# Kernel tuning notes

Measured on AMD Instinct MI355X. Metric: run time of the kernel, lower is better.

Reference implementation:

```python
import jax, jax.numpy as jnp
import numpy as np

B, SQ, SK = 2, 2048, 2048
D = 1024            # in_features == num_heads * head_size
H, HS = 16, 64      # num_heads, head_size
SCALE = HS ** -0.5


def setup_inputs() -> dict:
    key = jax.random.key(0)
    ks = jax.random.split(key, 10)
    s = 0.02
    return {
        "inputs": jax.random.normal(ks[0], (B, SQ, D), jnp.float32),
        "context": jax.random.normal(ks[1], (B, SK, D), jnp.float32),
        "Wq": jax.random.normal(ks[2], (D, D), jnp.float32) * s,
        "bq": jnp.zeros((D,), jnp.float32),
        "Wk": jax.random.normal(ks[3], (D, D), jnp.float32) * s,
        "bk": jnp.zeros((D,), jnp.float32),
        "Wv": jax.random.normal(ks[4], (D, D), jnp.float32) * s,
        "bv": jnp.zeros((D,), jnp.float32),
        "Wo": jax.random.normal(ks[5], (D, D), jnp.float32) * s,
        "bo": jnp.zeros((D,), jnp.float32),
    }


def reference(inputs, context, Wq, bq, Wk, bk, Wv, bv, Wo, bo):
    # QKV projections (torch Linear: x @ W.T + b; here W stored as [in, out])
    q = inputs @ Wq + bq            # [B, SQ, D]
    k = context @ Wk + bk           # [B, SK, D]
    v = context @ Wv + bv           # [B, SK, D]
    q = q.reshape(B, SQ, H, HS)
    k = k.reshape(B, SK, H, HS)
    v = v.reshape(B, SK, H, HS)
    # scores: [B, H, SQ, SK] -- full score matrix materialized (as in source)
    score = jnp.einsum("bqhd,bkhd->bhqk", q, k) * SCALE
    weights = jax.nn.softmax(score, axis=-1)
    attn = jnp.einsum("bhqk,bkhd->bqhd", weights, v)  # [B, SQ, H, HS]
    out = attn.reshape(B, SQ, H * HS)
    return out @ Wo + bo
```

## Files before the change

kernel.cpp:

```cpp
#include <hip/hip_runtime.h>

#define BB 2
#define SQ 2048
#define SK 2048
#define DD 1024
#define HH 16
#define HS 64
#define SCALE 0.125f
#define LOG2E 1.4426950408889634f

typedef __bf16 bf16x8 __attribute__((ext_vector_type(8)));
typedef float f32x4 __attribute__((ext_vector_type(4)));
typedef unsigned int uint;

#if defined(__has_builtin)
#if __has_builtin(__builtin_amdgcn_exp2f)
#define FEXP2(x) __builtin_amdgcn_exp2f(x)
#endif
#endif
#ifndef FEXP2
extern "C" __device__ float __ocml_native_exp2_f32(float);
#define FEXP2(x) __ocml_native_exp2_f32(x)
#endif

__device__ __forceinline__ void gload_lds16(const __bf16* g, __bf16* l) {
    __builtin_amdgcn_global_load_lds((const __attribute__((address_space(1))) uint*)(g),
                                     (__attribute__((address_space(3))) uint*)(l), 16, 0, 0);
}

__global__ void cast2_f32_bf16(const float* __restrict__ in0, const float* __restrict__ in1,
                               __bf16* __restrict__ out0, __bf16* __restrict__ out1, int n8each) {
    int i = blockIdx.x * blockDim.x + threadIdx.x;
    const float* src;
    __bf16* dst;
    int j;
    if (i < n8each) { src = in0; dst = out0; j = i; }
    else            { src = in1; dst = out1; j = i - n8each; }
    const float4* p = ((const float4*)src) + (size_t)j * 2;
    float4 a = p[0], b = p[1];
    bf16x8 v = {(__bf16)a.x, (__bf16)a.y, (__bf16)a.z, (__bf16)a.w,
                (__bf16)b.x, (__bf16)b.y, (__bf16)b.z, (__bf16)b.w};
    ((bf16x8*)dst)[j] = v;
}

__global__ void wtrans(const float* __restrict__ W0, const float* __restrict__ W1,
                       const float* __restrict__ W2, const float* __restrict__ W3,
                       __bf16* __restrict__ Wt) {
    __shared__ __bf16 tile[32][33];
    const float* W = blockIdx.z == 0 ? W0 : blockIdx.z == 1 ? W1 : blockIdx.z == 2 ? W2 : W3;
    __bf16* out = Wt + (size_t)blockIdx.z * DD * DD;
    int tx = threadIdx.x, ty = threadIdx.y;
    int k0 = blockIdx.y * 32, n0 = blockIdx.x * 32;
#pragma unroll
    for (int j = 0; j < 4; ++j)
        tile[ty + j * 8][tx] = (__bf16)W[(size_t)(k0 + ty + j * 8) * DD + n0 + tx];
    __syncthreads();
#pragma unroll
    for (int j = 0; j < 4; ++j) {
        int n = n0 + ty + j * 8;
        int k = k0 + tx;
        int kswz = (k & ~63) | ((((k >> 3) ^ n) & 7) << 3) | (k & 7);
        out[(size_t)n * DD + kswz] = tile[tx][ty + j * 8];
    }
}

__global__ __launch_bounds__(256) void gemm_qkv(
        const __bf16* __restrict__ Ain, const __bf16* __restrict__ Actx,
        const __bf16* __restrict__ Wt,
        const float* __restrict__ bq, const float* __restrict__ bk, const float* __restrict__ bv,
        __bf16* __restrict__ Qb, __bf16* __restrict__ Kb, __bf16* __restrict__ Vtb,
        float qscale) {
    __shared__ __bf16 As[128 * 64];
    __shared__ __bf16 Bs[128 * 64];
    int t = threadIdx.x, w = t >> 6, l = t & 63;
    int lm = l & 15, lk = l >> 4;
    int wr = w >> 1, wc = w & 1;
    int flat = blockIdx.x + 16 * blockIdx.y;
    int nf = (flat & 7) * 96 + (flat >> 3);
    bool isQ = nf < 256;
    int bc, br;
    if (isQ) { bc = nf & 7; br = nf >> 3; }
    else     { int f = nf - 256; bc = f & 15; br = f >> 4; }

    int rA = t >> 3, cA = t & 7;
    const __bf16* ag = (isQ ? Ain : Actx) + (size_t)(br * 128 + rA) * 1024 + ((cA ^ (rA & 7)) * 8);
    __bf16* adst = &As[rA * 64 + cA * 8];
    const __bf16 *bg0, *bg1, *bg2, *bg3;
    if (isQ) {
        const __bf16* Wq_ = Wt;
        bg0 = Wq_ + (size_t)(bc * 128 + rA)      * 1024 + cA * 8;
        bg1 = Wq_ + (size_t)(bc * 128 + rA + 32) * 1024 + cA * 8;
        bg2 = Wq_ + (size_t)(bc * 128 + rA + 64) * 1024 + cA * 8;
        bg3 = Wq_ + (size_t)(bc * 128 + rA + 96) * 1024 + cA * 8;
    } else {
        const __bf16* Wk_ = Wt + (size_t)DD * DD;
        const __bf16* Wv_ = Wt + (size_t)2 * DD * DD;
        bg0 = Wk_ + (size_t)(bc * 64 + rA)      * 1024 + cA * 8;
        bg1 = Wk_ + (size_t)(bc * 64 + rA + 32) * 1024 + cA * 8;
        bg2 = Wv_ + (size_t)(bc * 64 + rA)      * 1024 + cA * 8;
        bg3 = Wv_ + (size_t)(bc * 64 + rA + 32) * 1024 + cA * 8;
    }
    __bf16* bdst = &Bs[rA * 64 + cA * 8];

    int brow[4];
#pragma unroll
    for (int n = 0; n < 4; ++n)
        brow[n] = isQ ? (wc * 64 + n * 16 + lm)
                      : ((n >> 1) * 64 + wc * 32 + (n & 1) * 16 + lm);

#define STAGE(KT)                                                                     \
    gload_lds16(ag + (KT),               adst);                                       \
    gload_lds16(ag + 32768 + (KT),       adst + 2048);                                \
    gload_lds16(ag + 65536 + (KT),       adst + 4096);                                \
    gload_lds16(ag + 98304 + (KT),       adst + 6144);                                \
    gload_lds16(bg0 + (KT), bdst);                                                    \
    gload_lds16(bg1 + (KT), bdst + 2048);                                             \
    gload_lds16(bg2 + (KT), bdst + 4096);                                             \
    gload_lds16(bg3 + (KT), bdst + 6144);

    f32x4 acc[4][4] = {};
    for (int ts = 0; ts < 16; ++ts) {
        __syncthreads();
        STAGE(ts * 64);
        __syncthreads();
#pragma unroll
        for (int kk = 0; kk < 2; ++kk) {
            int ch = kk * 4 + lk;
            bf16x8 af[4], bf[4];
#pragma unroll
            for (int m = 0; m < 4; ++m)
                af[m] = *(const bf16x8*)&As[(wr * 64 + m * 16 + lm) * 64 + ((ch ^ (lm & 7)) * 8)];
#pragma unroll
            for (int n = 0; n < 4; ++n)
                bf[n] = *(const bf16x8*)&Bs[brow[n] * 64 + ((ch ^ (lm & 7)) * 8)];
#pragma unroll
            for (int m = 0; m < 4; ++m)
#pragma unroll
                for (int n = 0; n < 4; ++n)
                    acc[m][n] = __builtin_amdgcn_mfma_f32_16x16x32_bf16(af[m], bf[n], acc[m][n], 0, 0, 0);
        }
    }
#undef STAGE

    if (isQ) {
#pragma unroll
        for (int m = 0; m < 4; ++m)
#pragma unroll
            for (int n = 0; n < 4; ++n) {
                int col = bc * 128 + wc * 64 + n * 16 + lm;
                float bb = bq[col];
#pragma unroll
                for (int r = 0; r < 4; ++r) {
                    int row = br * 128 + wr * 64 + m * 16 + lk * 4 + r;
                    Qb[(size_t)row * 1024 + col] = (__bf16)((acc[m][n][r] + bb) * qscale);
                }
            }
    } else {
#pragma unroll
        for (int m = 0; m < 4; ++m)
#pragma unroll
            for (int n = 0; n < 4; ++n) {
                int col = bc * 64 + wc * 32 + (n & 1) * 16 + lm;
                if (n < 2) {
                    float bb = bk[col];
#pragma unroll
                    for (int r = 0; r < 4; ++r) {
                        int row = br * 128 + wr * 64 + m * 16 + lk * 4 + r;
                        Kb[(size_t)row * 1024 + col] = (__bf16)(acc[m][n][r] + bb);
                    }
                } else {
                    float bb = bv[col];
                    int row = br * 128 + wr * 64 + m * 16 + lk * 4;
                    int b_ = row >> 11, sk = row & 2047;
                    int skb = sk & ~63, o = sk & 63;
                    int p0 = (o & 32) | (((o >> 3) & 1) << 4) | (((o >> 2) & 1) << 3) | (((o >> 4) & 1) << 2);
                    int h_ = col >> 6, d_ = col & 63;
                    union { ushort4 u; __bf16 hh[4]; } pk;
#pragma unroll
                    for (int r = 0; r < 4; ++r) pk.hh[r] = (__bf16)(acc[m][n][r] + bb);
                    *(ushort4*)(Vtb + ((size_t)((b_ * 16 + h_) * 64 + d_) * 2048 + skb + p0)) = pk.u;
                }
            }
    }
}

__global__ __launch_bounds__(256) void gemm_out64(const __bf16* __restrict__ A, const __bf16* __restrict__ Bt,
                                                  const float* __restrict__ bias, float* __restrict__ C) {
    __shared__ __bf16 As[64][64];
    __shared__ __bf16 Bs[128][64];
    int t = threadIdx.x;
    int w = t >> 6, l = t & 63;
    int lm = l & 15, lk = l >> 4;
    int flat = blockIdx.x + 8 * blockIdx.y;
    int nf = (flat & 7) * 64 + (flat >> 3);
    int bc = nf & 7, br = nf >> 3;
    int srow = (l >> 3), scol = (l & 7) * 8;
    f32x4 acc[4][2] = {};
    for (int kt = 0; kt < 1024; kt += 64) {
        __syncthreads();
#pragma unroll
        for (int j = 0; j < 2; ++j) {
            int r0 = (j * 4 + w) * 8;
            gload_lds16(&A[(size_t)(br * 64 + r0 + srow) * 1024 + kt + scol], &As[r0][0]);
        }
#pragma unroll
        for (int j = 0; j < 4; ++j) {
            int r0 = (j * 4 + w) * 8;
            gload_lds16(&Bt[(size_t)(bc * 128 + r0 + srow) * 1024 + kt + scol], &Bs[r0][0]);
        }
        __syncthreads();
#pragma unroll
        for (int kk = 0; kk < 64; kk += 32) {
            int ch = ((kk >> 3) + lk);
            bf16x8 af[4], bf[2];
#pragma unroll
            for (int m = 0; m < 4; ++m) af[m] = *(const bf16x8*)&As[m * 16 + lm][kk + lk * 8];
#pragma unroll
            for (int n = 0; n < 2; ++n)
                bf[n] = *(const bf16x8*)&Bs[w * 32 + n * 16 + lm][(ch ^ (lm & 7)) * 8];
#pragma unroll
            for (int m = 0; m < 4; ++m)
#pragma unroll
                for (int n = 0; n < 2; ++n)
                    acc[m][n] = __builtin_amdgcn_mfma_f32_16x16x32_bf16(af[m], bf[n], acc[m][n], 0, 0, 0);
        }
    }
#pragma unroll
    for (int m = 0; m < 4; ++m)
#pragma unroll
        for (int n = 0; n < 2; ++n) {
            int col = bc * 128 + w * 32 + n * 16 + lm;
            float bv = bias[col];
#pragma unroll
            for (int r = 0; r < 4; ++r) {
                int row = br * 64 + m * 16 + lk * 4 + r;
                C[(size_t)row * 1024 + col] = acc[m][n][r] + bv;
            }
        }
}

__global__ __launch_bounds__(512) void flash_attn(const __bf16* __restrict__ Q,
                                                  const __bf16* __restrict__ Kb,
                                                  const __bf16* __restrict__ Vt,
                                                  __bf16* __restrict__ O) {
    __shared__ __bf16 Ks[2][64 * 64];
    __shared__ __bf16 Vs[2][64 * 64];
    int t = threadIdx.x, w = t >> 6, l = t & 63;
    int lm = l & 15, lk = l >> 4;
    int flat = blockIdx.x + 16 * blockIdx.y;
    int nf = (flat & 7) * 64 + (flat >> 3);
    int bh = nf >> 4, b = bh >> 4, h = bh & 15;
    int q0 = (nf & 15) * 128;

    bf16x8 qf[2];
#pragma unroll
    for (int kk = 0; kk < 2; ++kk)
        qf[kk] = *(const bf16x8*)&Q[(size_t)(b * SQ + q0 + w * 16 + lm) * DD + h * HS + kk * 32 + lk * 8];

    int r0 = t >> 3, c8 = t & 7;
    int chs = c8 ^ (r0 & 7);
    __bf16* ksl0 = &Ks[0][r0 * 64 + chs * 8];
    __bf16* vsl0 = &Vs[0][r0 * 64 + chs * 8];

    const __bf16* kp0 = Kb + (size_t)b * SK * DD + h * HS + (size_t)r0 * DD + c8 * 8;
    const __bf16* vp0 = Vt + (size_t)bh * HS * SK + (size_t)r0 * SK + c8 * 8;

    int o0 = lm * 64 + ((lk ^ (lm & 7)) * 8);
    int o1 = lm * 64 + (((4 + lk) ^ (lm & 7)) * 8);

    float4 kr0, vr0;
#define FA_LOAD()                                                                \
    kr0 = *(const float4*)kp0; vr0 = *(const float4*)vp0;                        \
    kp0 += (size_t)64 * DD; vp0 += 64;
#define FA_WRITE(BUF)                                                            \
    *(float4*)(ksl0 + (BUF) * 4096) = kr0;                                       \
    *(float4*)(vsl0 + (BUF) * 4096) = vr0;

    FA_LOAD();
    FA_WRITE(0);
    __syncthreads();

    bf16x8 ones;
#pragma unroll
    for (int j = 0; j < 8; ++j) ones[j] = (__bf16)1.0f;

    f32x4 o[4] = {};
    f32x4 o_s = {};

    for (int it = 0; it < 32; ++it) {
        int buf = it & 1;
        if (it + 1 < 32) { FA_LOAD(); }

        const __bf16* KsB = &Ks[buf][0];
        const __bf16* VsB = &Vs[buf][0];

        f32x4 st[4] = {};
        __builtin_amdgcn_s_setprio(1);
#pragma unroll
        for (int kk = 0; kk < 2; ++kk) {
#pragma unroll
            for (int n = 0; n < 4; ++n) {
                bf16x8 kf = *(const bf16x8*)&KsB[(kk ? o1 : o0) + n * 1024];
                st[n] = __builtin_amdgcn_mfma_f32_16x16x32_bf16(kf, qf[kk], st[n], 0, 0, 0);
            }
        }
        __builtin_amdgcn_s_setprio(0);

#pragma unroll
        for (int kk = 0; kk < 2; ++kk) {
            bf16x8 pa;
#pragma unroll
            for (int j = 0; j < 8; ++j)
                pa[j] = (__bf16)FEXP2(st[2 * kk + (j >> 2)][j & 3]);
            __builtin_amdgcn_s_setprio(1);
            o_s = __builtin_amdgcn_mfma_f32_16x16x32_bf16(pa, ones, o_s, 0, 0, 0);
#pragma unroll
            for (int dn = 0; dn < 4; ++dn) {
                bf16x8 vf = *(const bf16x8*)&VsB[(kk ? o1 : o0) + dn * 1024];
                o[dn] = __builtin_amdgcn_mfma_f32_16x16x32_bf16(pa, vf, o[dn], 0, 0, 0);
            }
            __builtin_amdgcn_s_setprio(0);
        }

        if (it + 1 < 32) { FA_WRITE(buf ^ 1); }
        __syncthreads();
    }

    f32x4 inv;
#pragma unroll
    for (int r = 0; r < 4; ++r) inv[r] = 1.f / o_s[r];
#pragma unroll
    for (int dn = 0; dn < 4; ++dn)
#pragma unroll
        for (int r = 0; r < 4; ++r) {
            int row = q0 + w * 16 + lk * 4 + r;
            int col = h * HS + dn * 16 + lm;
            O[(size_t)(b * SQ + row) * DD + col] = (__bf16)(o[dn][r] * inv[r]);
        }
}

extern "C" void kernel_launch(void* const* d_in, const int* in_sizes, int n_in,
                              void* d_out, int out_size, void* d_ws, size_t ws_size,
                              hipStream_t stream) {
    const float* inputs  = (const float*)d_in[0];
    const float* context = (const float*)d_in[1];
    const float* Wq = (const float*)d_in[2];
    const float* bq = (const float*)d_in[3];
    const float* Wk = (const float*)d_in[4];
    const float* bk = (const float*)d_in[5];
    const float* Wv = (const float*)d_in[6];
    const float* bv = (const float*)d_in[7];
    const float* Wo = (const float*)d_in[8];
    const float* bo = (const float*)d_in[9];
    float* out = (float*)d_out;

    char* ws = (char*)d_ws;
    const size_t SEG = (size_t)4096 * 1024 * sizeof(__bf16);
    __bf16* attb = (__bf16*)(ws + 0 * SEG);
    __bf16* inA  = (__bf16*)(ws + 1 * SEG);
    __bf16* Wt   = (__bf16*)(ws + 2 * SEG);
    __bf16* Qb   = (__bf16*)(ws + 3 * SEG);
    __bf16* Kbuf = (__bf16*)(ws + 4 * SEG);
    __bf16* Vtb  = (__bf16*)(ws + 5 * SEG);
    __bf16* ctxB = (__bf16*)(ws + 6 * SEG);

    int n8 = 4096 * 1024 / 8;
    cast2_f32_bf16<<<2 * n8 / 256, 256, 0, stream>>>(inputs, context, inA, ctxB, n8);
    wtrans<<<dim3(32, 32, 4), dim3(32, 8), 0, stream>>>(Wq, Wk, Wv, Wo, Wt);

    gemm_qkv<<<dim3(16, 48), 256, 0, stream>>>(inA, ctxB, Wt, bq, bk, bv,
                                               Qb, Kbuf, Vtb, SCALE * LOG2E);

    flash_attn<<<dim3(16, 32), 512, 0, stream>>>(Qb, Kbuf, Vtb, attb);

    gemm_out64<<<dim3(8, 64), 256, 0, stream>>>(attb, Wt + (size_t)3 * DD * DD, bo, out);
}
```

Baseline: 118.0 us.

## Double-buffer LDS tiles in QKV and output GEMMs; grid-stride cast kernel

```diff
diff --git a/kernel.cpp b/kernel.cpp
--- a/kernel.cpp
+++ b/kernel.cpp
@@ -30,17 +30,19 @@
 
 __global__ void cast2_f32_bf16(const float* __restrict__ in0, const float* __restrict__ in1,
                                __bf16* __restrict__ out0, __bf16* __restrict__ out1, int n8each) {
-    int i = blockIdx.x * blockDim.x + threadIdx.x;
-    const float* src;
-    __bf16* dst;
-    int j;
-    if (i < n8each) { src = in0; dst = out0; j = i; }
-    else            { src = in1; dst = out1; j = i - n8each; }
-    const float4* p = ((const float4*)src) + (size_t)j * 2;
-    float4 a = p[0], b = p[1];
-    bf16x8 v = {(__bf16)a.x, (__bf16)a.y, (__bf16)a.z, (__bf16)a.w,
-                (__bf16)b.x, (__bf16)b.y, (__bf16)b.z, (__bf16)b.w};
-    ((bf16x8*)dst)[j] = v;
+    int stride = gridDim.x * blockDim.x;
+    for (int i = blockIdx.x * blockDim.x + threadIdx.x; i < 2 * n8each; i += stride) {
+        const float* src;
+        __bf16* dst;
+        int j;
+        if (i < n8each) { src = in0; dst = out0; j = i; }
+        else            { src = in1; dst = out1; j = i - n8each; }
+        const float4* p = ((const float4*)src) + (size_t)j * 2;
+        float4 a = p[0], b = p[1];
+        bf16x8 v = {(__bf16)a.x, (__bf16)a.y, (__bf16)a.z, (__bf16)a.w,
+                    (__bf16)b.x, (__bf16)b.y, (__bf16)b.z, (__bf16)b.w};
+        ((bf16x8*)dst)[j] = v;
+    }
 }
 
 __global__ void wtrans(const float* __restrict__ W0, const float* __restrict__ W1,
@@ -70,8 +72,8 @@
         const float* __restrict__ bq, const float* __restrict__ bk, const float* __restrict__ bv,
         __bf16* __restrict__ Qb, __bf16* __restrict__ Kb, __bf16* __restrict__ Vtb,
         float qscale) {
-    __shared__ __bf16 As[128 * 64];
-    __shared__ __bf16 Bs[128 * 64];
+    __shared__ __bf16 As[2 * 128 * 64];
+    __shared__ __bf16 Bs[2 * 128 * 64];
     int t = threadIdx.x, w = t >> 6, l = t & 63;
     int lm = l & 15, lk = l >> 4;
     int wr = w >> 1, wc = w & 1;
@@ -108,37 +110,39 @@
         brow[n] = isQ ? (wc * 64 + n * 16 + lm)
                       : ((n >> 1) * 64 + wc * 32 + (n & 1) * 16 + lm);
 
-#define STAGE(KT)                                                                     \
-    gload_lds16(ag + (KT),               adst);                                       \
-    gload_lds16(ag + 32768 + (KT),       adst + 2048);                                \
-    gload_lds16(ag + 65536 + (KT),       adst + 4096);                                \
-    gload_lds16(ag + 98304 + (KT),       adst + 6144);                                \
-    gload_lds16(bg0 + (KT), bdst);                                                    \
-    gload_lds16(bg1 + (KT), bdst + 2048);                                             \
-    gload_lds16(bg2 + (KT), bdst + 4096);                                             \
-    gload_lds16(bg3 + (KT), bdst + 6144);
+#define STAGE(BUF, KT)                                                                \
+    gload_lds16(ag + (KT),               adst + (BUF) * 8192);                        \
+    gload_lds16(ag + 32768 + (KT),       adst + (BUF) * 8192 + 2048);                 \
+    gload_lds16(ag + 65536 + (KT),       adst + (BUF) * 8192 + 4096);                 \
+    gload_lds16(ag + 98304 + (KT),       adst + (BUF) * 8192 + 6144);                 \
+    gload_lds16(bg0 + (KT), bdst + (BUF) * 8192);                                     \
+    gload_lds16(bg1 + (KT), bdst + (BUF) * 8192 + 2048);                              \
+    gload_lds16(bg2 + (KT), bdst + (BUF) * 8192 + 4096);                              \
+    gload_lds16(bg3 + (KT), bdst + (BUF) * 8192 + 6144);
 
     f32x4 acc[4][4] = {};
+    STAGE(0, 0);
+    __syncthreads();
     for (int ts = 0; ts < 16; ++ts) {
-        __syncthreads();
-        STAGE(ts * 64);
-        __syncthreads();
+        int buf = ts & 1;
+        if (ts + 1 < 16) { STAGE(buf ^ 1, (ts + 1) * 64); }
 #pragma unroll
         for (int kk = 0; kk < 2; ++kk) {
             int ch = kk * 4 + lk;
             bf16x8 af[4], bf[4];
 #pragma unroll
             for (int m = 0; m < 4; ++m)
-                af[m] = *(const bf16x8*)&As[(wr * 64 + m * 16 + lm) * 64 + ((ch ^ (lm & 7)) * 8)];
+                af[m] = *(const bf16x8*)&As[buf * 8192 + (wr * 64 + m * 16 + lm) * 64 + ((ch ^ (lm & 7)) * 8)];
 #pragma unroll
             for (int n = 0; n < 4; ++n)
-                bf[n] = *(const bf16x8*)&Bs[brow[n] * 64 + ((ch ^ (lm & 7)) * 8)];
+                bf[n] = *(const bf16x8*)&Bs[buf * 8192 + brow[n] * 64 + ((ch ^ (lm & 7)) * 8)];
 #pragma unroll
             for (int m = 0; m < 4; ++m)
 #pragma unroll
                 for (int n = 0; n < 4; ++n)
                     acc[m][n] = __builtin_amdgcn_mfma_f32_16x16x32_bf16(af[m], bf[n], acc[m][n], 0, 0, 0);
         }
+        __syncthreads();
     }
 #undef STAGE
 
@@ -186,45 +190,54 @@
 
 __global__ __launch_bounds__(256) void gemm_out64(const __bf16* __restrict__ A, const __bf16* __restrict__ Bt,
                                                   const float* __restrict__ bias, float* __restrict__ C) {
-    __shared__ __bf16 As[64][64];
-    __shared__ __bf16 Bs[128][64];
+    __shared__ __bf16 As[2 * 64 * 64];
+    __shared__ __bf16 Bs[2 * 128 * 64];
     int t = threadIdx.x;
     int w = t >> 6, l = t & 63;
     int lm = l & 15, lk = l >> 4;
     int flat = blockIdx.x + 8 * blockIdx.y;
     int nf = (flat & 7) * 64 + (flat >> 3);
     int bc = nf & 7, br = nf >> 3;
-    int srow = (l >> 3), scol = (l & 7) * 8;
+
+    int rA = t >> 3, cA = t & 7;
+    const __bf16* as0 = A + (size_t)(br * 64 + rA) * 1024 + cA * 8;
+    __bf16* adst = &As[rA * 64 + cA * 8];
+    const __bf16* bs0 = Bt + (size_t)(bc * 128 + rA) * 1024 + cA * 8;
+    __bf16* bdst = &Bs[rA * 64 + cA * 8];
+
+#define STAGE(BUF, KT)                                                                \
+    gload_lds16(as0 + (KT),             adst + (BUF) * 4096);                         \
+    gload_lds16(as0 + 32768 + (KT),     adst + (BUF) * 4096 + 2048);                  \
+    gload_lds16(bs0 + (KT),             bdst + (BUF) * 8192);                         \
+    gload_lds16(bs0 + 32768 + (KT),     bdst + (BUF) * 8192 + 2048);                  \
+    gload_lds16(bs0 + 65536 + (KT),     bdst + (BUF) * 8192 + 4096);                  \
+    gload_lds16(bs0 + 98304 + (KT),     bdst + (BUF) * 8192 + 6144);
+
     f32x4 acc[4][2] = {};
-    for (int kt = 0; kt < 1024; kt += 64) {
-        __syncthreads();
-#pragma unroll
-        for (int j = 0; j < 2; ++j) {
-            int r0 = (j * 4 + w) * 8;
-            gload_lds16(&A[(size_t)(br * 64 + r0 + srow) * 1024 + kt + scol], &As[r0][0]);
-        }
-#pragma unroll
-        for (int j = 0; j < 4; ++j) {
-            int r0 = (j * 4 + w) * 8;
-            gload_lds16(&Bt[(size_t)(bc * 128 + r0 + srow) * 1024 + kt + scol], &Bs[r0][0]);
-        }
-        __syncthreads();
-#pragma unroll
-        for (int kk = 0; kk < 64; kk += 32) {
-            int ch = ((kk >> 3) + lk);
+    STAGE(0, 0);
+    __syncthreads();
+    for (int ts = 0; ts < 16; ++ts) {
+        int buf = ts & 1;
+        if (ts + 1 < 16) { STAGE(buf ^ 1, (ts + 1) * 64); }
+#pragma unroll
+        for (int kk = 0; kk < 2; ++kk) {
+            int ch = kk * 4 + lk;
             bf16x8 af[4], bf[2];
 #pragma unroll
-            for (int m = 0; m < 4; ++m) af[m] = *(const bf16x8*)&As[m * 16 + lm][kk + lk * 8];
+            for (int m = 0; m < 4; ++m)
+                af[m] = *(const bf16x8*)&As[buf * 4096 + (m * 16 + lm) * 64 + (kk * 32 + lk * 8)];
 #pragma unroll
             for (int n = 0; n < 2; ++n)
-                bf[n] = *(const bf16x8*)&Bs[w * 32 + n * 16 + lm][(ch ^ (lm & 7)) * 8];
+                bf[n] = *(const bf16x8*)&Bs[buf * 8192 + (w * 32 + n * 16 + lm) * 64 + ((ch ^ (lm & 7)) * 8)];
 #pragma unroll
             for (int m = 0; m < 4; ++m)
 #pragma unroll
                 for (int n = 0; n < 2; ++n)
                     acc[m][n] = __builtin_amdgcn_mfma_f32_16x16x32_bf16(af[m], bf[n], acc[m][n], 0, 0, 0);
         }
-    }
+        __syncthreads();
+    }
+#undef STAGE
 #pragma unroll
     for (int m = 0; m < 4; ++m)
 #pragma unroll
@@ -365,7 +378,7 @@
     __bf16* ctxB = (__bf16*)(ws + 6 * SEG);
 
     int n8 = 4096 * 1024 / 8;
-    cast2_f32_bf16<<<2 * n8 / 256, 256, 0, stream>>>(inputs, context, inA, ctxB, n8);
+    cast2_f32_bf16<<<2048, 256, 0, stream>>>(inputs, context, inA, ctxB, n8);
     wtrans<<<dim3(32, 32, 4), dim3(32, 8), 0, stream>>>(Wq, Wk, Wv, Wo, Wt);
 
     gemm_qkv<<<dim3(16, 48), 256, 0, stream>>>(inA, ctxB, Wt, bq, bk, bv,
```

Result: slower. 120.7 us (+2.3%).
